# Kernel optimization log

Measured on AMD Instinct MI355X. Metric: run time of the kernel, lower is better.

## Reference

```python
import jax, jax.numpy as jnp
import numpy as np

M = 20000   # users
N = 20000   # items
E = 320000  # edges per channel per direction
C = 4       # channels
H = 4       # attention heads
D_IN = 256
D_OUT = 128
NEG_SLOPE = 0.01  # F.leaky_relu default


def setup_inputs() -> dict:
    key = jax.random.key(0)
    ks = jax.random.split(key, 12)
    u_prev = jax.random.normal(ks[0], (M, D_IN), jnp.float32)
    i_prev = jax.random.normal(ks[1], (N, D_IN), jnp.float32)
    # raw (pre-cumsum) shared parameters, 0.1*randn as in the module
    w_user = 0.1 * jax.random.normal(ks[2], (C, D_IN, D_OUT), jnp.float32)
    w_item = 0.1 * jax.random.normal(ks[3], (C, D_IN, D_OUT), jnp.float32)
    a_u_src = 0.1 * jax.random.normal(ks[4], (H, C, D_OUT), jnp.float32)
    a_u_dst = 0.1 * jax.random.normal(ks[5], (H, C, D_OUT), jnp.float32)
    a_i_src = 0.1 * jax.random.normal(ks[6], (H, C, D_OUT), jnp.float32)
    a_i_dst = 0.1 * jax.random.normal(ks[7], (H, C, D_OUT), jnp.float32)
    u2i_row = jax.random.randint(ks[8], (C, E), 0, M, jnp.int32)
    u2i_col = jax.random.randint(ks[9], (C, E), 0, N, jnp.int32)
    i2u_row = jax.random.randint(ks[10], (C, E), 0, N, jnp.int32)
    i2u_col = jax.random.randint(ks[11], (C, E), 0, M, jnp.int32)
    return dict(u_prev=u_prev, i_prev=i_prev, w_user=w_user, w_item=w_item,
                a_u_src=a_u_src, a_u_dst=a_u_dst, a_i_src=a_i_src, a_i_dst=a_i_dst,
                u2i_row=u2i_row, u2i_col=u2i_col, i2u_row=i2u_row, i2u_col=i2u_col)


def _segment_softmax(logits, seg, num_segments):
    # neighborhood softmax over edges grouped by destination row
    mx = jax.ops.segment_max(logits, seg, num_segments=num_segments)
    ex = jnp.exp(logits - mx[seg])
    den = jax.ops.segment_sum(ex, seg, num_segments=num_segments)
    return ex / den[seg]


def _attend(row, col, h_src, h_dst, a_src, a_dst, n_rows):
    # a_src, a_dst: (H, D_OUT). reduce_att = sum over heads; inner nonlinear = identity.
    # Node-level scores first (equivalent to gathering then dotting, much cheaper).
    s_src = h_src @ a_src.T  # (m, H)
    s_dst = h_dst @ a_dst.T  # (n, H)
    out = jnp.zeros((n_rows, h_dst.shape[1]), h_dst.dtype)
    for j in range(a_src.shape[0]):  # fixed small head loop
        logits = jax.nn.leaky_relu(s_src[row, j] + s_dst[col, j], NEG_SLOPE)  # (E,)
        att = _segment_softmax(logits, row, n_rows)                            # (E,)
        # sparse-dense matmul: out[r] += att_e * h_dst[c]
        out = out + jax.ops.segment_sum(att[:, None] * h_dst[col], row, num_segments=n_rows)
    return out


def reference(u_prev, i_prev, w_user, w_item, a_u_src, a_u_dst, a_i_src, a_i_dst,
              u2i_row, u2i_col, i2u_row, i2u_col):
    # SharedParameter[idx] = sum(xs[:idx+1]) -> cumulative sum along channel axis
    Wu = jnp.cumsum(w_user, axis=0)   # (C, D_IN, D_OUT)
    Wi = jnp.cumsum(w_item, axis=0)
    Aus = jnp.cumsum(a_u_src, axis=1)  # (H, C, D_OUT)
    Aud = jnp.cumsum(a_u_dst, axis=1)
    Ais = jnp.cumsum(a_i_src, axis=1)
    Aid = jnp.cumsum(a_i_dst, axis=1)

    u_outs, i_outs = [], []
    for c in range(C):
        u = u_prev @ Wu[c]  # (M, D_OUT), bias = 0 in MCGATLayer
        i = i_prev @ Wi[c]  # (N, D_OUT)
        u_next = _attend(u2i_row[c], u2i_col[c], u, i, Aus[:, c], Aud[:, c], M)
        i_next = _attend(i2u_row[c], i2u_col[c], i, u, Ais[:, c], Aid[:, c], N)
        u_outs.append(u_next)
        i_outs.append(i_next)

    # reduce_chnl == 'cat' (uniq_i = all nodes -> index_copy is identity placement)
    u_final = jax.nn.relu(jnp.concatenate(u_outs, axis=1))  # (M, C*D_OUT)
    i_final = jax.nn.relu(jnp.concatenate(i_outs, axis=1))  # (N, C*D_OUT)
    return (u_final, i_final)
```

## Files before the change

### kernel.cpp

```cpp
#include <hip/hip_runtime.h>
#include <math.h>

#define M_NODES 20000
#define MPAD    20096
#define NE      320000
#define NC      4
#define NH      4
#define DIN     256
#define DOUT    128
#define DCAT    512

#define RPB   256
#define NBKT  79
#define EPB   2048
#define NBLK  157
#define CAP   8192

typedef __attribute__((ext_vector_type(8))) _Float16 half8v;
typedef __attribute__((ext_vector_type(2))) _Float16 half2v;
typedef __attribute__((ext_vector_type(4))) float f32x4;

__device__ __forceinline__ unsigned short f2h(float x) {
    _Float16 h = (_Float16)x;
    return __builtin_bit_cast(unsigned short, h);
}
__device__ __forceinline__ void gload16(const void* g, void* l) {
    __builtin_amdgcn_global_load_lds(
        (const __attribute__((address_space(1))) void*)g,
        (__attribute__((address_space(3))) void*)l,
        16, 0, 0);
}

__global__ __launch_bounds__(256) void k_prep(const float* __restrict__ u_prev, const float* __restrict__ i_prev,
                                              const float* __restrict__ w_user, const float* __restrict__ w_item,
                                              const float* __restrict__ a_u_src, const float* __restrict__ a_u_dst,
                                              const float* __restrict__ a_i_src, const float* __restrict__ a_i_dst,
                                              const int* __restrict__ u2i_row, const int* __restrict__ i2u_row,
                                              unsigned short* __restrict__ AbU, unsigned short* __restrict__ AbI,
                                              unsigned short* __restrict__ BTu, unsigned short* __restrict__ BTi,
                                              unsigned short* __restrict__ Bvec, int* __restrict__ cnt3) {
    __shared__ int hist[NBKT];
    int bid = blockIdx.x, tid = threadIdx.x;
    if (bid < 5000) {
        int sideI = bid >= 2500;
        int t = (sideI ? bid - 2500 : bid) * 256 + tid;
        int row = t >> 5, kc = (t & 31) * 8;
        const float* src = sideI ? i_prev : u_prev;
        unsigned short* dst = sideI ? AbI : AbU;
        float4 x0 = *(const float4*)(src + (size_t)row * DIN + kc);
        float4 x1 = *(const float4*)(src + (size_t)row * DIN + kc + 4);
        float xs[8] = {x0.x, x0.y, x0.z, x0.w, x1.x, x1.y, x1.z, x1.w};
        unsigned int H[4];
#pragma unroll
        for (int p = 0; p < 4; ++p)
            H[p] = (unsigned int)f2h(xs[2 * p]) | ((unsigned int)f2h(xs[2 * p + 1]) << 16);
        *(uint4*)(dst + (size_t)row * 256 + kc) = make_uint4(H[0], H[1], H[2], H[3]);
        return;
    }
    if (bid < 6256) {
        int sub = bid - 5000;
        int combo = sub / NBLK, blk = sub % NBLK;
        int c = combo >> 1, dir = combo & 1;
        const int* rows = (dir ? i2u_row : u2i_row) + (size_t)c * NE;
        if (tid < NBKT) hist[tid] = 0;
        __syncthreads();
        int e0 = blk * EPB + tid * 8;
        if (e0 + 8 <= NE) {
            int4 r0 = *(const int4*)(rows + e0);
            int4 r1 = *(const int4*)(rows + e0 + 4);
            atomicAdd(&hist[r0.x >> 8], 1); atomicAdd(&hist[r0.y >> 8], 1);
            atomicAdd(&hist[r0.z >> 8], 1); atomicAdd(&hist[r0.w >> 8], 1);
            atomicAdd(&hist[r1.x >> 8], 1); atomicAdd(&hist[r1.y >> 8], 1);
            atomicAdd(&hist[r1.z >> 8], 1); atomicAdd(&hist[r1.w >> 8], 1);
        }
        __syncthreads();
        if (tid < NBKT) cnt3[((size_t)combo * NBKT + tid) * NBLK + blk] = hist[tid];
        return;
    }
    if (bid < 6384) {
        int idx = (bid - 6256) * 256 + tid;
        int k = idx >> 7, j = idx & 127;
        float su = 0.f, si = 0.f;
        for (int c = 0; c < NC; ++c) {
            su += w_user[((size_t)c * DIN + k) * DOUT + j];
            si += w_item[((size_t)c * DIN + k) * DOUT + j];
            size_t n = (size_t)(c * DOUT + j) * 256;
            BTu[n + k] = f2h(su);
            BTi[n + k] = f2h(si);
        }
        return;
    }
    {
        int t = (bid - 6384) * 256 + tid;
        int lane = t & 63, ks = (t >> 6) & 3, c = (t >> 8) & 3, side = t >> 10;
        int col = lane & 15, g = lane >> 4;
        int kind = (col >> 2) & 1, h = col & 3;
        const float* araw = kind ? (side ? a_u_dst : a_i_dst) : (side ? a_i_src : a_u_src);
        unsigned int out2[4];
#pragma unroll
        for (int p = 0; p < 4; ++p) {
            unsigned short e2[2];
#pragma unroll
            for (int q = 0; q < 2; ++q) {
                int j = p * 2 + q;
                int kdim = ks * 32 + g * 8 + j;
                float s = 0.f;
                if (col < 8)
                    for (int c2 = 0; c2 <= c; ++c2) s += araw[(h * NC + c2) * DOUT + kdim];
                e2[q] = f2h(s);
            }
            out2[p] = (unsigned int)e2[0] | ((unsigned int)e2[1] << 16);
        }
        *(uint4*)(Bvec + ((size_t)(((side * 4 + c) * 4 + ks) * 64 + lane)) * 8) =
            make_uint4(out2[0], out2[1], out2[2], out2[3]);
    }
}

__global__ __launch_bounds__(256) void k_gmm(const unsigned short* __restrict__ AbU,
                                             const unsigned short* __restrict__ AbI,
                                             const unsigned short* __restrict__ BTu,
                                             const unsigned short* __restrict__ BTi,
                                             const unsigned short* __restrict__ Bvec,
                                             unsigned short* __restrict__ fbu,
                                             unsigned short* __restrict__ fbi,
                                             float* __restrict__ su_src, float* __restrict__ su_dst,
                                             float* __restrict__ si_src, float* __restrict__ si_dst,
                                             int* __restrict__ cnt3, int* __restrict__ btot,
                                             int* __restrict__ bbase) {
    __shared__ unsigned short As[128 * 64];
    __shared__ unsigned short Bs[128 * 64];
    __shared__ int tot[128];
    int bid = blockIdx.x, tid = threadIdx.x;
    if (bid < 1256) {
        int side = bid >= 628;
        int t = side ? bid - 628 : bid;
        int c = t / 157, mb = t % 157;
        const unsigned short* Ab = side ? AbI : AbU;
        const unsigned short* BT = side ? BTi : BTu;
        unsigned short* fb       = side ? fbi : fbu;
        int m0 = mb * 128;
        int w = tid >> 6, lane = tid & 63;
        int wrb = (w >> 1) * 64, wcb = (w & 1) * 64;
        int l15 = lane & 15, g = lane >> 4;
        int srow = lane >> 3, scol = (lane & 7) * 8;
        f32x4 acc[4][4] = {};
        for (int kt = 0; kt < 4; ++kt) {
            int k0 = kt * 64;
#pragma unroll
            for (int tt = 0; tt < 4; ++tt) {
                int chunk = w * 4 + tt;
                int row8 = chunk * 8 + srow;
                gload16(Ab + (size_t)(m0 + row8) * 256 + k0 + scol, (char*)As + chunk * 1024);
                gload16(BT + (size_t)(c * 128 + row8) * 256 + k0 + scol, (char*)Bs + chunk * 1024);
            }
            __syncthreads();
#pragma unroll
            for (int ks = 0; ks < 2; ++ks) {
                half8v a[4], b[4];
#pragma unroll
                for (int i = 0; i < 4; ++i)
                    a[i] = *(const half8v*)(&As[(wrb + i * 16 + l15) * 64 + ks * 32 + g * 8]);
#pragma unroll
                for (int j = 0; j < 4; ++j)
                    b[j] = *(const half8v*)(&Bs[(wcb + j * 16 + l15) * 64 + ks * 32 + g * 8]);
#pragma unroll
                for (int i = 0; i < 4; ++i)
#pragma unroll
                    for (int j = 0; j < 4; ++j)
                        acc[i][j] = __builtin_amdgcn_mfma_f32_16x16x32_f16(a[i], b[j], acc[i][j], 0, 0, 0);
            }
            __syncthreads();
        }
#pragma unroll
        for (int i = 0; i < 4; ++i) {
#pragma unroll
            for (int r = 0; r < 4; ++r) {
                int nl = wrb + i * 16 + g * 4 + r;
                int node = m0 + nl;
                bool valid = node < M_NODES;
#pragma unroll
                for (int j = 0; j < 4; ++j) {
                    int d = wcb + j * 16 + l15;
                    unsigned short hv = f2h(acc[i][j][r]);
                    if (valid) fb[((size_t)c * M_NODES + node) * DOUT + d] = hv;
                    if (d < 64) As[nl * 64 + d] = hv;
                    else        Bs[nl * 64 + (d - 64)] = hv;
                }
            }
        }
        __syncthreads();
        {
            half8v bv[4];
#pragma unroll
            for (int ks = 0; ks < 4; ++ks)
                bv[ks] = *(const half8v*)(Bvec + ((size_t)(((side * 4 + c) * 4 + ks) * 64 + lane)) * 8);
#pragma unroll
            for (int mt2 = 0; mt2 < 2; ++mt2) {
                int mt = w * 2 + mt2;
                f32x4 sacc = {};
#pragma unroll
                for (int ks = 0; ks < 4; ++ks) {
                    int nl = mt * 16 + l15;
                    const unsigned short* base = (ks < 2) ? As : Bs;
                    half8v a = *(const half8v*)(&base[nl * 64 + (ks & 1) * 32 + g * 8]);
                    sacc = __builtin_amdgcn_mfma_f32_16x16x32_f16(a, bv[ks], sacc, 0, 0, 0);
                }
                int col = l15;
                if (col < 8) {
                    int kind = col >> 2, h = col & 3;
                    float* dst = kind ? (side ? si_dst : su_dst) : (side ? si_src : su_src);
#pragma unroll
                    for (int r = 0; r < 4; ++r) {
                        int node = m0 + mt * 16 + g * 4 + r;
                        if (node < M_NODES)
                            dst[((size_t)c * M_NODES + node) * 4 + h] = sacc[r];
                    }
                }
            }
        }
        return;
    }
    {
        int combo = bid - 1256;
        if (tid < NBKT) {
            size_t base = ((size_t)combo * NBKT + tid) * NBLK;
            int run = 0;
            for (int b = 0; b < NBLK; ++b) {
                int v = cnt3[base + b];
                cnt3[base + b] = run;
                run += v;
            }
            tot[tid] = run;
            btot[combo * NBKT + tid] = run;
        }
        __syncthreads();
        if (tid < 64) {
            int carry = 0;
            for (int ch = 0; ch < 2; ++ch) {
                int idx = ch * 64 + tid;
                int v = (idx < NBKT) ? tot[idx] : 0;
                int inc = v;
                for (int o = 1; o < 64; o <<= 1) {
                    int tv = __shfl_up(inc, o);
                    if (tid >= o) inc += tv;
                }
                if (idx < NBKT) bbase[combo * NBKT + idx] = carry + inc - v;
                carry += __shfl(inc, 63);
            }
        }
    }
}

__global__ __launch_bounds__(256) void k_bfill(const int* __restrict__ u2i_row, const int* __restrict__ u2i_col,
                                               const int* __restrict__ i2u_row, const int* __restrict__ i2u_col,
                                               const int* __restrict__ cnt3, const int* __restrict__ bbase,
                                               unsigned int* __restrict__ pairbuf) {
    __shared__ int cur[NBKT];
    int bid = blockIdx.x, tid = threadIdx.x;
    int combo = bid / NBLK, blk = bid % NBLK;
    int c = combo >> 1, dir = combo & 1;
    const int* rows = (dir ? i2u_row : u2i_row) + (size_t)c * NE;
    const int* cols = (dir ? i2u_col : u2i_col) + (size_t)c * NE;
    if (tid < NBKT)
        cur[tid] = bbase[combo * NBKT + tid] + cnt3[((size_t)combo * NBKT + tid) * NBLK + blk];
    __syncthreads();
    unsigned int* pb = pairbuf + (size_t)combo * NE;
    int e0 = blk * EPB + tid * 8;
    if (e0 + 8 <= NE) {
        int4 r0 = *(const int4*)(rows + e0);
        int4 r1 = *(const int4*)(rows + e0 + 4);
        int4 c0 = *(const int4*)(cols + e0);
        int4 c1 = *(const int4*)(cols + e0 + 4);
        int rr[8] = {r0.x, r0.y, r0.z, r0.w, r1.x, r1.y, r1.z, r1.w};
        int cc[8] = {c0.x, c0.y, c0.z, c0.w, c1.x, c1.y, c1.z, c1.w};
#pragma unroll
        for (int k = 0; k < 8; ++k) {
            int pos = atomicAdd(&cur[rr[k] >> 8], 1);
            pb[pos] = ((unsigned int)rr[k] << 16) | (unsigned int)cc[k];
        }
    }
}

__global__ __launch_bounds__(256) void k_finalize(const unsigned int* __restrict__ pairbuf,
                                                  const int* __restrict__ bbase, const int* __restrict__ btot,
                                                  int* __restrict__ csroff, int* __restrict__ csrcol) {
    __shared__ int hist[RPB];
    __shared__ int cur[RPB];
    __shared__ int lcol[CAP];
    int tid = threadIdx.x, bkt = blockIdx.x, combo = blockIdx.y;
    int base = bbase[combo * NBKT + bkt];
    int cntb = btot[combo * NBKT + bkt];
    const unsigned int* pb = pairbuf + (size_t)combo * NE + base;
    int* ccol = csrcol + (size_t)combo * NE + base;
    hist[tid] = 0;
    __syncthreads();
    for (int k = tid; k < cntb; k += 256)
        atomicAdd(&hist[(pb[k] >> 16) & (RPB - 1)], 1);
    __syncthreads();
    for (int st = 1; st < RPB; st <<= 1) {
        int v = (tid >= st) ? hist[tid - st] : 0;
        __syncthreads();
        hist[tid] += v;
        __syncthreads();
    }
    int ex = (tid == 0) ? 0 : hist[tid - 1];
    cur[tid] = ex;
    int row = bkt * RPB + tid;
    if (row < M_NODES) csroff[combo * (M_NODES + 1) + row] = base + ex;
    if (bkt == NBKT - 1 && tid == 0) csroff[combo * (M_NODES + 1) + M_NODES] = NE;
    __syncthreads();
    for (int k = tid; k < cntb; k += 256) {
        unsigned int p = pb[k];
        int rl  = (p >> 16) & (RPB - 1);
        int col = (int)(p & 0xffffu);
        int pos = atomicAdd(&cur[rl], 1);
        if (pos < CAP) lcol[pos] = col; else ccol[pos] = col;
    }
    __syncthreads();
    int lim = min(cntb, CAP);
    for (int k = tid; k < lim; k += 256) ccol[k] = lcol[k];
}

__device__ void attend_row_wave(int r, int s0, int deg, const float* __restrict__ ssrc,
                                const float* __restrict__ sdst, const unsigned short* __restrict__ fbd,
                                const int* __restrict__ co, float* __restrict__ o, int lane) {
    if (deg <= 64) {
        float w = 0.f;
        int cl = 0;
        if (deg > 0) {
            float4 ssv = *(const float4*)(ssrc + (size_t)r * 4);
            float ss[4] = {ssv.x, ssv.y, ssv.z, ssv.w};
            float lg[4];
            if (lane < deg) {
                cl = co[s0 + lane];
                float4 sdv = *(const float4*)(sdst + (size_t)cl * 4);
                float sd[4] = {sdv.x, sdv.y, sdv.z, sdv.w};
#pragma unroll
                for (int h = 0; h < 4; ++h) {
                    float x = ss[h] + sd[h];
                    lg[h] = x > 0.f ? x : 0.01f * x;
                }
            } else {
#pragma unroll
                for (int h = 0; h < 4; ++h) lg[h] = -1e30f;
            }
            float ex[4], den[4];
#pragma unroll
            for (int h = 0; h < 4; ++h) {
                ex[h] = __expf(fminf(lg[h], 80.f));
                den[h] = ex[h];
            }
#pragma unroll
            for (int h = 0; h < 4; ++h)
                for (int o2 = 32; o2; o2 >>= 1) den[h] += __shfl_xor(den[h], o2);
#pragma unroll
            for (int h = 0; h < 4; ++h) w += ex[h] * (1.f / den[h]);
        }
        int q = lane >> 4, l16 = lane & 15;
        const unsigned short* fbl = fbd + l16 * 8;
        float a8[8] = {};
        for (int j = 0; j < deg; j += 4) {
            int e = j + q;
            float we = __shfl(w, e & 63);
            int   ce = __shfl(cl, e & 63);
            if (e < deg) {
                half8v v = *(const half8v*)(fbl + (size_t)ce * DOUT);
#pragma unroll
                for (int k = 0; k < 8; ++k) a8[k] = fmaf(we, (float)v[k], a8[k]);
            }
        }
#pragma unroll
        for (int i = 0; i < 8; ++i) {
            a8[i] += __shfl_xor(a8[i], 16);
            a8[i] += __shfl_xor(a8[i], 32);
        }
        if (lane < 16) {
            float4 r0 = make_float4(fmaxf(a8[0], 0.f), fmaxf(a8[1], 0.f), fmaxf(a8[2], 0.f), fmaxf(a8[3], 0.f));
            float4 r1 = make_float4(fmaxf(a8[4], 0.f), fmaxf(a8[5], 0.f), fmaxf(a8[6], 0.f), fmaxf(a8[7], 0.f));
            *(float4*)(o + l16 * 8) = r0;
            *(float4*)(o + l16 * 8 + 4) = r1;
        }
        return;
    }
    float acc0 = 0.f, acc1 = 0.f;
    {
        float4 ssv = *(const float4*)(ssrc + (size_t)r * 4);
        float ss[4] = {ssv.x, ssv.y, ssv.z, ssv.w};
        float den[4] = {0.f, 0.f, 0.f, 0.f};
        for (int base = 0; base < deg; base += 64) {
            int e = base + lane;
            float ex[4] = {0.f, 0.f, 0.f, 0.f};
            if (e < deg) {
                int cl = co[s0 + e];
                float4 sdv = *(const float4*)(sdst + (size_t)cl * 4);
                float sd[4] = {sdv.x, sdv.y, sdv.z, sdv.w};
#pragma unroll
                for (int h = 0; h < 4; ++h) {
                    float x = ss[h] + sd[h];
                    x = x > 0.f ? x : 0.01f * x;
                    ex[h] = __expf(fminf(x, 80.f));
                }
            }
#pragma unroll
            for (int h = 0; h < 4; ++h) {
                float v = ex[h];
                for (int o2 = 32; o2; o2 >>= 1) v += __shfl_xor(v, o2);
                den[h] += v;
            }
        }
        float inv[4];
#pragma unroll
        for (int h = 0; h < 4; ++h) inv[h] = 1.f / den[h];
        for (int base = 0; base < deg; base += 64) {
            int e = base + lane;
            float w = 0.f;
            int cl = 0;
            if (e < deg) {
                cl = co[s0 + e];
                float4 sdv = *(const float4*)(sdst + (size_t)cl * 4);
                float sd[4] = {sdv.x, sdv.y, sdv.z, sdv.w};
#pragma unroll
                for (int h = 0; h < 4; ++h) {
                    float x = ss[h] + sd[h];
                    x = x > 0.f ? x : 0.01f * x;
                    w += __expf(fminf(x, 80.f)) * inv[h];
                }
            }
            int cnt2 = min(64, deg - base);
            for (int j = 0; j < cnt2; ++j) {
                float wj = __shfl(w, j);
                int   cj = __shfl(cl, j);
                half2v hv = *(const half2v*)(fbd + (size_t)cj * DOUT + lane * 2);
                acc0 = fmaf(wj, (float)hv[0], acc0);
                acc1 = fmaf(wj, (float)hv[1], acc1);
            }
        }
    }
    o[lane * 2]     = fmaxf(acc0, 0.f);
    o[lane * 2 + 1] = fmaxf(acc1, 0.f);
}

__global__ __launch_bounds__(256) void k_attend(const unsigned short* __restrict__ fbu, const unsigned short* __restrict__ fbi,
                                                const float* __restrict__ su_src, const float* __restrict__ su_dst,
                                                const float* __restrict__ si_src, const float* __restrict__ si_dst,
                                                const int* __restrict__ off, const int* __restrict__ cols,
                                                float* __restrict__ out) {
    int bid = blockIdx.x;
    int combo = bid & 7, c = combo >> 1, dir = combo & 1;
    int wavein = threadIdx.x >> 6, lane = threadIdx.x & 63;
    int half = lane >> 5, l = lane & 31;
    int rbase = (bid >> 3) * 8 + wavein * 2;
    const float* ssrc = (dir ? si_src : su_src) + (size_t)c * M_NODES * NH;
    const float* sdst = (dir ? su_dst : si_dst) + (size_t)c * M_NODES * NH;
    const unsigned short* fbd = (dir ? fbu : fbi) + (size_t)c * M_NODES * DOUT;
    const int* co = cols + (size_t)combo * NE;
    const int* offc = off + combo * (M_NODES + 1);
    int r = rbase + half;
    int s0 = offc[r];
    int deg = offc[r + 1] - s0;
    int degmax = max(deg, __shfl_xor(deg, 32));
    float* o = out + ((size_t)(dir ? M_NODES + r : r)) * DCAT + c * DOUT;

    if (degmax <= 32) {
        unsigned int pk = 0;
        if (deg > 0) {
            float w = 0.f;
            int cl = 0;
            float4 ssv = *(const float4*)(ssrc + (size_t)r * 4);
            float ss[4] = {ssv.x, ssv.y, ssv.z, ssv.w};
            float lg[4];
            if (l < deg) {
                cl = co[s0 + l];
                float4 sdv = *(const float4*)(sdst + (size_t)cl * 4);
                float sd[4] = {sdv.x, sdv.y, sdv.z, sdv.w};
#pragma unroll
                for (int h = 0; h < 4; ++h) {
                    float x = ss[h] + sd[h];
                    lg[h] = x > 0.f ? x : 0.01f * x;
                }
            } else {
#pragma unroll
                for (int h = 0; h < 4; ++h) lg[h] = -1e30f;
            }
            float ex[4], den[4];
#pragma unroll
            for (int h = 0; h < 4; ++h) {
                ex[h] = __expf(fminf(lg[h], 80.f));
                den[h] = ex[h];
            }
#pragma unroll
            for (int h = 0; h < 4; ++h)
                for (int o2 = 16; o2; o2 >>= 1) den[h] += __shfl_xor(den[h], o2);
#pragma unroll
            for (int h = 0; h < 4; ++h) w += ex[h] * (1.f / den[h]);
            pk = ((unsigned int)f2h(w) << 16) | (unsigned int)(cl & 0xffff);
        }
        int q2 = (l >> 4), l16 = l & 15;
        const char* fc = (const char*)(fbd + l16 * 8);
        half8v ah = {};
        int hb = half * 32;
        int j = 0;
        for (; j + 8 <= deg; j += 8) {
            unsigned int p0 = __shfl(pk, hb + j + q2);
            unsigned int p1 = __shfl(pk, hb + j + 2 + q2);
            unsigned int p2 = __shfl(pk, hb + j + 4 + q2);
            unsigned int p3 = __shfl(pk, hb + j + 6 + q2);
            half8v v0 = *(const half8v*)(fc + ((size_t)(p0 & 0xffffu) << 8));
            half8v v1 = *(const half8v*)(fc + ((size_t)(p1 & 0xffffu) << 8));
            half8v v2 = *(const half8v*)(fc + ((size_t)(p2 & 0xffffu) << 8));
            half8v v3 = *(const half8v*)(fc + ((size_t)(p3 & 0xffffu) << 8));
            ah += v0 * __builtin_bit_cast(_Float16, (unsigned short)(p0 >> 16));
            ah += v1 * __builtin_bit_cast(_Float16, (unsigned short)(p1 >> 16));
            ah += v2 * __builtin_bit_cast(_Float16, (unsigned short)(p2 >> 16));
            ah += v3 * __builtin_bit_cast(_Float16, (unsigned short)(p3 >> 16));
        }
        for (; j < deg; j += 4) {
            int e0 = j + q2, e1 = j + 2 + q2;
            unsigned int p0 = __shfl(pk, hb + min(e0, 31));
            unsigned int p1 = __shfl(pk, hb + min(e1, 31));
            p0 = (e0 < deg) ? p0 : 0u;
            p1 = (e1 < deg) ? p1 : 0u;
            half8v v0 = *(const half8v*)(fc + ((size_t)(p0 & 0xffffu) << 8));
            half8v v1 = *(const half8v*)(fc + ((size_t)(p1 & 0xffffu) << 8));
            ah += v0 * __builtin_bit_cast(_Float16, (unsigned short)(p0 >> 16));
            ah += v1 * __builtin_bit_cast(_Float16, (unsigned short)(p1 >> 16));
        }
        int4 ui = __builtin_bit_cast(int4, ah);
        int4 uo;
        uo.x = __shfl_xor(ui.x, 16);
        uo.y = __shfl_xor(ui.y, 16);
        uo.z = __shfl_xor(ui.z, 16);
        uo.w = __shfl_xor(ui.w, 16);
        ah += __builtin_bit_cast(half8v, uo);
        if (l < 16) {
            float4 r0 = make_float4(fmaxf((float)ah[0], 0.f), fmaxf((float)ah[1], 0.f),
                                    fmaxf((float)ah[2], 0.f), fmaxf((float)ah[3], 0.f));
            float4 r1 = make_float4(fmaxf((float)ah[4], 0.f), fmaxf((float)ah[5], 0.f),
                                    fmaxf((float)ah[6], 0.f), fmaxf((float)ah[7], 0.f));
            *(float4*)(o + l16 * 8) = r0;
            *(float4*)(o + l16 * 8 + 4) = r1;
        }
        return;
    }

    for (int rr = 0; rr < 2; ++rr) {
        int r2 = rbase + rr;
        int t0 = offc[r2];
        int d2 = offc[r2 + 1] - t0;
        float* o2 = out + ((size_t)(dir ? M_NODES + r2 : r2)) * DCAT + c * DOUT;
        attend_row_wave(r2, t0, d2, ssrc, sdst, fbd, co, o2, lane);
    }
}

extern "C" void kernel_launch(void* const* d_in, const int* in_sizes, int n_in,
                              void* d_out, int out_size, void* d_ws, size_t ws_size,
                              hipStream_t stream) {
    const float* u_prev  = (const float*)d_in[0];
    const float* i_prev  = (const float*)d_in[1];
    const float* w_user  = (const float*)d_in[2];
    const float* w_item  = (const float*)d_in[3];
    const float* a_u_src = (const float*)d_in[4];
    const float* a_u_dst = (const float*)d_in[5];
    const float* a_i_src = (const float*)d_in[6];
    const float* a_i_dst = (const float*)d_in[7];
    const int* u2i_row = (const int*)d_in[8];
    const int* u2i_col = (const int*)d_in[9];
    const int* i2u_row = (const int*)d_in[10];
    const int* i2u_col = (const int*)d_in[11];
    float* out = (float*)d_out;

    char* ws = (char*)d_ws;
    size_t woff = 0;
    auto alloc = [&](size_t bytes) -> char* {
        char* p = ws + woff;
        woff += (bytes + 255) & ~(size_t)255;
        return p;
    };
    unsigned short* AbU   = (unsigned short*)alloc((size_t)MPAD * 256 * 2);
    unsigned short* AbI   = (unsigned short*)alloc((size_t)MPAD * 256 * 2);
    unsigned short* BTu   = (unsigned short*)alloc((size_t)512 * 256 * 2);
    unsigned short* BTi   = (unsigned short*)alloc((size_t)512 * 256 * 2);
    unsigned short* Bvec  = (unsigned short*)alloc((size_t)2 * 4 * 4 * 64 * 8 * 2);
    unsigned short* fbu   = (unsigned short*)alloc((size_t)NC * M_NODES * DOUT * 2);
    unsigned short* fbi   = (unsigned short*)alloc((size_t)NC * M_NODES * DOUT * 2);
    float* su_src = (float*)alloc((size_t)NC * M_NODES * NH * 4);
    float* su_dst = (float*)alloc((size_t)NC * M_NODES * NH * 4);
    float* si_src = (float*)alloc((size_t)NC * M_NODES * NH * 4);
    float* si_dst = (float*)alloc((size_t)NC * M_NODES * NH * 4);
    int* csroff   = (int*)alloc((size_t)8 * (M_NODES + 1) * 4);
    int* csrcol   = (int*)alloc((size_t)8 * NE * 4);
    int* cnt3     = (int*)alloc((size_t)8 * NBKT * NBLK * 4);
    int* btot     = (int*)alloc((size_t)8 * NBKT * 4);
    int* bbase    = (int*)alloc((size_t)8 * NBKT * 4);
    unsigned int* pairbuf = (unsigned int*)alloc((size_t)8 * NE * 4);

    k_prep<<<6392, 256, 0, stream>>>(u_prev, i_prev, w_user, w_item,
                                     a_u_src, a_u_dst, a_i_src, a_i_dst,
                                     u2i_row, i2u_row,
                                     AbU, AbI, BTu, BTi, Bvec, cnt3);
    k_gmm<<<1264, 256, 0, stream>>>(AbU, AbI, BTu, BTi, Bvec, fbu, fbi,
                                    su_src, su_dst, si_src, si_dst,
                                    cnt3, btot, bbase);
    k_bfill<<<1256, 256, 0, stream>>>(u2i_row, u2i_col, i2u_row, i2u_col,
                                      cnt3, bbase, pairbuf);
    k_finalize<<<dim3(NBKT, 8), 256, 0, stream>>>(pairbuf, bbase, btot, csroff, csrcol);
    k_attend<<<dim3(M_NODES * 8 / 8), 256, 0, stream>>>(fbu, fbi, su_src, su_dst,
                                                        si_src, si_dst, csroff, csrcol, out);
}
```

Before: 143.3 us.

## Fuse CSR finalize into attention kernel with smaller row buckets held in LDS

Shrinks the row buckets from 256 to 64 rows, giving 313 buckets, and merges the finalize and attend kernels into one. Each block now builds its bucket's per-row column lists in shared memory and runs attention directly from LDS, so the csroff/csrcol arrays are never written to or read back from global memory. This removes one launch and a round-trip through global memory. The costs are more histogram buckets and scan work in the earlier kernels, and any bucket with more than 4096 edges would lose the overflowing columns because there is no spill path.

```diff
diff --git a/kernel.cpp b/kernel.cpp
--- a/kernel.cpp
+++ b/kernel.cpp
@@ -10,11 +10,11 @@
 #define DOUT    128
 #define DCAT    512
 
-#define RPB   256
-#define NBKT  79
+#define RPB2  64
+#define NBKT2 313
 #define EPB   2048
 #define NBLK  157
-#define CAP   8192
+#define CAP2  4096
 
 typedef __attribute__((ext_vector_type(8))) _Float16 half8v;
 typedef __attribute__((ext_vector_type(2))) _Float16 half2v;
@@ -39,7 +39,7 @@
                                               unsigned short* __restrict__ AbU, unsigned short* __restrict__ AbI,
                                               unsigned short* __restrict__ BTu, unsigned short* __restrict__ BTi,
                                               unsigned short* __restrict__ Bvec, int* __restrict__ cnt3) {
-    __shared__ int hist[NBKT];
+    __shared__ int hist[NBKT2];
     int bid = blockIdx.x, tid = threadIdx.x;
     if (bid < 5000) {
         int sideI = bid >= 2500;
@@ -62,19 +62,20 @@
         int combo = sub / NBLK, blk = sub % NBLK;
         int c = combo >> 1, dir = combo & 1;
         const int* rows = (dir ? i2u_row : u2i_row) + (size_t)c * NE;
-        if (tid < NBKT) hist[tid] = 0;
+        for (int i = tid; i < NBKT2; i += 256) hist[i] = 0;
         __syncthreads();
         int e0 = blk * EPB + tid * 8;
         if (e0 + 8 <= NE) {
             int4 r0 = *(const int4*)(rows + e0);
             int4 r1 = *(const int4*)(rows + e0 + 4);
-            atomicAdd(&hist[r0.x >> 8], 1); atomicAdd(&hist[r0.y >> 8], 1);
-            atomicAdd(&hist[r0.z >> 8], 1); atomicAdd(&hist[r0.w >> 8], 1);
-            atomicAdd(&hist[r1.x >> 8], 1); atomicAdd(&hist[r1.y >> 8], 1);
-            atomicAdd(&hist[r1.z >> 8], 1); atomicAdd(&hist[r1.w >> 8], 1);
+            atomicAdd(&hist[r0.x >> 6], 1); atomicAdd(&hist[r0.y >> 6], 1);
+            atomicAdd(&hist[r0.z >> 6], 1); atomicAdd(&hist[r0.w >> 6], 1);
+            atomicAdd(&hist[r1.x >> 6], 1); atomicAdd(&hist[r1.y >> 6], 1);
+            atomicAdd(&hist[r1.z >> 6], 1); atomicAdd(&hist[r1.w >> 6], 1);
         }
         __syncthreads();
-        if (tid < NBKT) cnt3[((size_t)combo * NBKT + tid) * NBLK + blk] = hist[tid];
+        for (int i = tid; i < NBKT2; i += 256)
+            cnt3[((size_t)combo * NBKT2 + i) * NBLK + blk] = hist[i];
         return;
     }
     if (bid < 6384) {
@@ -129,7 +130,7 @@
                                              int* __restrict__ bbase) {
     __shared__ unsigned short As[128 * 64];
     __shared__ unsigned short Bs[128 * 64];
-    __shared__ int tot[128];
+    __shared__ int tot[NBKT2];
     int bid = blockIdx.x, tid = threadIdx.x;
     if (bid < 1256) {
         int side = bid >= 628;
@@ -222,29 +223,29 @@
     }
     {
         int combo = bid - 1256;
-        if (tid < NBKT) {
-            size_t base = ((size_t)combo * NBKT + tid) * NBLK;
+        for (int bkt = tid; bkt < NBKT2; bkt += 256) {
+            size_t basep = ((size_t)combo * NBKT2 + bkt) * NBLK;
             int run = 0;
             for (int b = 0; b < NBLK; ++b) {
-                int v = cnt3[base + b];
-                cnt3[base + b] = run;
+                int v = cnt3[basep + b];
+                cnt3[basep + b] = run;
                 run += v;
             }
-            tot[tid] = run;
-            btot[combo * NBKT + tid] = run;
+            tot[bkt] = run;
+            btot[combo * NBKT2 + bkt] = run;
         }
         __syncthreads();
         if (tid < 64) {
             int carry = 0;
-            for (int ch = 0; ch < 2; ++ch) {
+            for (int ch = 0; ch < 5; ++ch) {
                 int idx = ch * 64 + tid;
-                int v = (idx < NBKT) ? tot[idx] : 0;
+                int v = (idx < NBKT2) ? tot[idx] : 0;
                 int inc = v;
                 for (int o = 1; o < 64; o <<= 1) {
                     int tv = __shfl_up(inc, o);
                     if (tid >= o) inc += tv;
                 }
-                if (idx < NBKT) bbase[combo * NBKT + idx] = carry + inc - v;
+                if (idx < NBKT2) bbase[combo * NBKT2 + idx] = carry + inc - v;
                 carry += __shfl(inc, 63);
             }
         }
@@ -255,14 +256,14 @@
                                                const int* __restrict__ i2u_row, const int* __restrict__ i2u_col,
                                                const int* __restrict__ cnt3, const int* __restrict__ bbase,
                                                unsigned int* __restrict__ pairbuf) {
-    __shared__ int cur[NBKT];
+    __shared__ int cur[NBKT2];
     int bid = blockIdx.x, tid = threadIdx.x;
     int combo = bid / NBLK, blk = bid % NBLK;
     int c = combo >> 1, dir = combo & 1;
     const int* rows = (dir ? i2u_row : u2i_row) + (size_t)c * NE;
     const int* cols = (dir ? i2u_col : u2i_col) + (size_t)c * NE;
-    if (tid < NBKT)
-        cur[tid] = bbase[combo * NBKT + tid] + cnt3[((size_t)combo * NBKT + tid) * NBLK + blk];
+    for (int i = tid; i < NBKT2; i += 256)
+        cur[i] = bbase[combo * NBKT2 + i] + cnt3[((size_t)combo * NBKT2 + i) * NBLK + blk];
     __syncthreads();
     unsigned int* pb = pairbuf + (size_t)combo * NE;
     int e0 = blk * EPB + tid * 8;
@@ -275,55 +276,15 @@
         int cc[8] = {c0.x, c0.y, c0.z, c0.w, c1.x, c1.y, c1.z, c1.w};
 #pragma unroll
         for (int k = 0; k < 8; ++k) {
-            int pos = atomicAdd(&cur[rr[k] >> 8], 1);
+            int pos = atomicAdd(&cur[rr[k] >> 6], 1);
             pb[pos] = ((unsigned int)rr[k] << 16) | (unsigned int)cc[k];
         }
     }
-}
-
-__global__ __launch_bounds__(256) void k_finalize(const unsigned int* __restrict__ pairbuf,
-                                                  const int* __restrict__ bbase, const int* __restrict__ btot,
-                                                  int* __restrict__ csroff, int* __restrict__ csrcol) {
-    __shared__ int hist[RPB];
-    __shared__ int cur[RPB];
-    __shared__ int lcol[CAP];
-    int tid = threadIdx.x, bkt = blockIdx.x, combo = blockIdx.y;
-    int base = bbase[combo * NBKT + bkt];
-    int cntb = btot[combo * NBKT + bkt];
-    const unsigned int* pb = pairbuf + (size_t)combo * NE + base;
-    int* ccol = csrcol + (size_t)combo * NE + base;
-    hist[tid] = 0;
-    __syncthreads();
-    for (int k = tid; k < cntb; k += 256)
-        atomicAdd(&hist[(pb[k] >> 16) & (RPB - 1)], 1);
-    __syncthreads();
-    for (int st = 1; st < RPB; st <<= 1) {
-        int v = (tid >= st) ? hist[tid - st] : 0;
-        __syncthreads();
-        hist[tid] += v;
-        __syncthreads();
-    }
-    int ex = (tid == 0) ? 0 : hist[tid - 1];
-    cur[tid] = ex;
-    int row = bkt * RPB + tid;
-    if (row < M_NODES) csroff[combo * (M_NODES + 1) + row] = base + ex;
-    if (bkt == NBKT - 1 && tid == 0) csroff[combo * (M_NODES + 1) + M_NODES] = NE;
-    __syncthreads();
-    for (int k = tid; k < cntb; k += 256) {
-        unsigned int p = pb[k];
-        int rl  = (p >> 16) & (RPB - 1);
-        int col = (int)(p & 0xffffu);
-        int pos = atomicAdd(&cur[rl], 1);
-        if (pos < CAP) lcol[pos] = col; else ccol[pos] = col;
-    }
-    __syncthreads();
-    int lim = min(cntb, CAP);
-    for (int k = tid; k < lim; k += 256) ccol[k] = lcol[k];
 }
 
 __device__ void attend_row_wave(int r, int s0, int deg, const float* __restrict__ ssrc,
                                 const float* __restrict__ sdst, const unsigned short* __restrict__ fbd,
-                                const int* __restrict__ co, float* __restrict__ o, int lane) {
+                                const int* co, float* __restrict__ o, int lane) {
     if (deg <= 64) {
         float w = 0.f;
         int cl = 0;
@@ -440,115 +401,148 @@
     o[lane * 2 + 1] = fmaxf(acc1, 0.f);
 }
 
-__global__ __launch_bounds__(256) void k_attend(const unsigned short* __restrict__ fbu, const unsigned short* __restrict__ fbi,
-                                                const float* __restrict__ su_src, const float* __restrict__ su_dst,
-                                                const float* __restrict__ si_src, const float* __restrict__ si_dst,
-                                                const int* __restrict__ off, const int* __restrict__ cols,
-                                                float* __restrict__ out) {
-    int bid = blockIdx.x;
-    int combo = bid & 7, c = combo >> 1, dir = combo & 1;
-    int wavein = threadIdx.x >> 6, lane = threadIdx.x & 63;
-    int half = lane >> 5, l = lane & 31;
-    int rbase = (bid >> 3) * 8 + wavein * 2;
+__global__ __launch_bounds__(256) void k_fat(const unsigned int* __restrict__ pairbuf,
+                                             const int* __restrict__ bbase, const int* __restrict__ btot,
+                                             const unsigned short* __restrict__ fbu,
+                                             const unsigned short* __restrict__ fbi,
+                                             const float* __restrict__ su_src, const float* __restrict__ su_dst,
+                                             const float* __restrict__ si_src, const float* __restrict__ si_dst,
+                                             float* __restrict__ out) {
+    __shared__ int hist[RPB2];
+    __shared__ int cur[RPB2];
+    __shared__ int lcol[CAP2];
+    int tid = threadIdx.x, bid = blockIdx.x;
+    int combo = bid & 7, bkt = bid >> 3;
+    int c = combo >> 1, dir = combo & 1;
+    int base = bbase[combo * NBKT2 + bkt];
+    int cntb = btot[combo * NBKT2 + bkt];
+    const unsigned int* pb = pairbuf + (size_t)combo * NE + base;
+    if (tid < RPB2) hist[tid] = 0;
+    __syncthreads();
+    for (int k = tid; k < cntb; k += 256)
+        atomicAdd(&hist[(pb[k] >> 16) & (RPB2 - 1)], 1);
+    __syncthreads();
+    if (tid < 64) {
+        int v = hist[tid];
+        int inc = v;
+        for (int o = 1; o < 64; o <<= 1) {
+            int t = __shfl_up(inc, o);
+            if (tid >= o) inc += t;
+        }
+        hist[tid] = inc;
+        cur[tid] = inc - v;
+    }
+    __syncthreads();
+    for (int k = tid; k < cntb; k += 256) {
+        unsigned int p = pb[k];
+        int rl  = (p >> 16) & (RPB2 - 1);
+        int pos = atomicAdd(&cur[rl], 1);
+        if (pos < CAP2) lcol[pos] = (int)(p & 0xffffu);
+    }
+    __syncthreads();
     const float* ssrc = (dir ? si_src : su_src) + (size_t)c * M_NODES * NH;
     const float* sdst = (dir ? su_dst : si_dst) + (size_t)c * M_NODES * NH;
     const unsigned short* fbd = (dir ? fbu : fbi) + (size_t)c * M_NODES * DOUT;
-    const int* co = cols + (size_t)combo * NE;
-    const int* offc = off + combo * (M_NODES + 1);
-    int r = rbase + half;
-    int s0 = offc[r];
-    int deg = offc[r + 1] - s0;
-    int degmax = max(deg, __shfl_xor(deg, 32));
-    float* o = out + ((size_t)(dir ? M_NODES + r : r)) * DCAT + c * DOUT;
-
-    if (degmax <= 32) {
-        unsigned int pk = 0;
-        if (deg > 0) {
-            float w = 0.f;
-            int cl = 0;
-            float4 ssv = *(const float4*)(ssrc + (size_t)r * 4);
-            float ss[4] = {ssv.x, ssv.y, ssv.z, ssv.w};
-            float lg[4];
-            if (l < deg) {
-                cl = co[s0 + l];
-                float4 sdv = *(const float4*)(sdst + (size_t)cl * 4);
-                float sd[4] = {sdv.x, sdv.y, sdv.z, sdv.w};
+    int wavein = tid >> 6, lane = tid & 63;
+    int half = lane >> 5, l = lane & 31;
+    for (int iter = 0; iter < 8; ++iter) {
+        int rloc = iter * 8 + wavein * 2 + half;
+        int r = bkt * RPB2 + rloc;
+        int start = rloc ? hist[rloc - 1] : 0;
+        int deg = hist[rloc] - start;
+        int degmax = max(deg, __shfl_xor(deg, 32));
+        bool valid = r < M_NODES;
+        float* o = out + ((size_t)(dir ? M_NODES + r : r)) * DCAT + c * DOUT;
+        if (degmax <= 32) {
+            unsigned int pk = 0;
+            if (deg > 0) {
+                float w = 0.f;
+                int cl = 0;
+                float4 ssv = *(const float4*)(ssrc + (size_t)r * 4);
+                float ss[4] = {ssv.x, ssv.y, ssv.z, ssv.w};
+                float lg[4];
+                if (l < deg) {
+                    cl = lcol[start + l];
+                    float4 sdv = *(const float4*)(sdst + (size_t)cl * 4);
+                    float sd[4] = {sdv.x, sdv.y, sdv.z, sdv.w};
+#pragma unroll
+                    for (int h = 0; h < 4; ++h) {
+                        float x = ss[h] + sd[h];
+                        lg[h] = x > 0.f ? x : 0.01f * x;
+                    }
+                } else {
+#pragma unroll
+                    for (int h = 0; h < 4; ++h) lg[h] = -1e30f;
+                }
+                float ex[4], den[4];
 #pragma unroll
                 for (int h = 0; h < 4; ++h) {
-                    float x = ss[h] + sd[h];
-                    lg[h] = x > 0.f ? x : 0.01f * x;
-                }
-            } else {
-#pragma unroll
-                for (int h = 0; h < 4; ++h) lg[h] = -1e30f;
-            }
-            float ex[4], den[4];
-#pragma unroll
-            for (int h = 0; h < 4; ++h) {
-                ex[h] = __expf(fminf(lg[h], 80.f));
-                den[h] = ex[h];
-            }
-#pragma unroll
-            for (int h = 0; h < 4; ++h)
-                for (int o2 = 16; o2; o2 >>= 1) den[h] += __shfl_xor(den[h], o2);
-#pragma unroll
-            for (int h = 0; h < 4; ++h) w += ex[h] * (1.f / den[h]);
-            pk = ((unsigned int)f2h(w) << 16) | (unsigned int)(cl & 0xffff);
-        }
-        int q2 = (l >> 4), l16 = l & 15;
-        const char* fc = (const char*)(fbd + l16 * 8);
-        half8v ah = {};
-        int hb = half * 32;
-        int j = 0;
-        for (; j + 8 <= deg; j += 8) {
-            unsigned int p0 = __shfl(pk, hb + j + q2);
-            unsigned int p1 = __shfl(pk, hb + j + 2 + q2);
-            unsigned int p2 = __shfl(pk, hb + j + 4 + q2);
-            unsigned int p3 = __shfl(pk, hb + j + 6 + q2);
-            half8v v0 = *(const half8v*)(fc + ((size_t)(p0 & 0xffffu) << 8));
-            half8v v1 = *(const half8v*)(fc + ((size_t)(p1 & 0xffffu) << 8));
-            half8v v2 = *(const half8v*)(fc + ((size_t)(p2 & 0xffffu) << 8));
-            half8v v3 = *(const half8v*)(fc + ((size_t)(p3 & 0xffffu) << 8));
-            ah += v0 * __builtin_bit_cast(_Float16, (unsigned short)(p0 >> 16));
-            ah += v1 * __builtin_bit_cast(_Float16, (unsigned short)(p1 >> 16));
-            ah += v2 * __builtin_bit_cast(_Float16, (unsigned short)(p2 >> 16));
-            ah += v3 * __builtin_bit_cast(_Float16, (unsigned short)(p3 >> 16));
-        }
-        for (; j < deg; j += 4) {
-            int e0 = j + q2, e1 = j + 2 + q2;
-            unsigned int p0 = __shfl(pk, hb + min(e0, 31));
-            unsigned int p1 = __shfl(pk, hb + min(e1, 31));
-            p0 = (e0 < deg) ? p0 : 0u;
-            p1 = (e1 < deg) ? p1 : 0u;
-            half8v v0 = *(const half8v*)(fc + ((size_t)(p0 & 0xffffu) << 8));
-            half8v v1 = *(const half8v*)(fc + ((size_t)(p1 & 0xffffu) << 8));
-            ah += v0 * __builtin_bit_cast(_Float16, (unsigned short)(p0 >> 16));
-            ah += v1 * __builtin_bit_cast(_Float16, (unsigned short)(p1 >> 16));
-        }
-        int4 ui = __builtin_bit_cast(int4, ah);
-        int4 uo;
-        uo.x = __shfl_xor(ui.x, 16);
-        uo.y = __shfl_xor(ui.y, 16);
-        uo.z = __shfl_xor(ui.z, 16);
-        uo.w = __shfl_xor(ui.w, 16);
-        ah += __builtin_bit_cast(half8v, uo);
-        if (l < 16) {
-            float4 r0 = make_float4(fmaxf((float)ah[0], 0.f), fmaxf((float)ah[1], 0.f),
-                                    fmaxf((float)ah[2], 0.f), fmaxf((float)ah[3], 0.f));
-            float4 r1 = make_float4(fmaxf((float)ah[4], 0.f), fmaxf((float)ah[5], 0.f),
-                                    fmaxf((float)ah[6], 0.f), fmaxf((float)ah[7], 0.f));
-            *(float4*)(o + l16 * 8) = r0;
-            *(float4*)(o + l16 * 8 + 4) = r1;
-        }
-        return;
-    }
-
-    for (int rr = 0; rr < 2; ++rr) {
-        int r2 = rbase + rr;
-        int t0 = offc[r2];
-        int d2 = offc[r2 + 1] - t0;
-        float* o2 = out + ((size_t)(dir ? M_NODES + r2 : r2)) * DCAT + c * DOUT;
-        attend_row_wave(r2, t0, d2, ssrc, sdst, fbd, co, o2, lane);
+                    ex[h] = __expf(fminf(lg[h], 80.f));
+                    den[h] = ex[h];
+                }
+#pragma unroll
+                for (int h = 0; h < 4; ++h)
+                    for (int o2 = 16; o2; o2 >>= 1) den[h] += __shfl_xor(den[h], o2);
+#pragma unroll
+                for (int h = 0; h < 4; ++h) w += ex[h] * (1.f / den[h]);
+                pk = ((unsigned int)f2h(w) << 16) | (unsigned int)(cl & 0xffff);
+            }
+            int q2 = (l >> 4), l16 = l & 15;
+            const char* fc = (const char*)(fbd + l16 * 8);
+            half8v ah = {};
+            int hb = half * 32;
+            int j = 0;
+            for (; j + 8 <= deg; j += 8) {
+                unsigned int p0 = __shfl(pk, hb + j + q2);
+                unsigned int p1 = __shfl(pk, hb + j + 2 + q2);
+                unsigned int p2 = __shfl(pk, hb + j + 4 + q2);
+                unsigned int p3 = __shfl(pk, hb + j + 6 + q2);
+                half8v v0 = *(const half8v*)(fc + ((size_t)(p0 & 0xffffu) << 8));
+                half8v v1 = *(const half8v*)(fc + ((size_t)(p1 & 0xffffu) << 8));
+                half8v v2 = *(const half8v*)(fc + ((size_t)(p2 & 0xffffu) << 8));
+                half8v v3 = *(const half8v*)(fc + ((size_t)(p3 & 0xffffu) << 8));
+                ah += v0 * __builtin_bit_cast(_Float16, (unsigned short)(p0 >> 16));
+                ah += v1 * __builtin_bit_cast(_Float16, (unsigned short)(p1 >> 16));
+                ah += v2 * __builtin_bit_cast(_Float16, (unsigned short)(p2 >> 16));
+                ah += v3 * __builtin_bit_cast(_Float16, (unsigned short)(p3 >> 16));
+            }
+            for (; j < deg; j += 4) {
+                int e0 = j + q2, e1 = j + 2 + q2;
+                unsigned int p0 = __shfl(pk, hb + min(e0, 31));
+                unsigned int p1 = __shfl(pk, hb + min(e1, 31));
+                p0 = (e0 < deg) ? p0 : 0u;
+                p1 = (e1 < deg) ? p1 : 0u;
+                half8v v0 = *(const half8v*)(fc + ((size_t)(p0 & 0xffffu) << 8));
+                half8v v1 = *(const half8v*)(fc + ((size_t)(p1 & 0xffffu) << 8));
+                ah += v0 * __builtin_bit_cast(_Float16, (unsigned short)(p0 >> 16));
+                ah += v1 * __builtin_bit_cast(_Float16, (unsigned short)(p1 >> 16));
+            }
+            int4 ui = __builtin_bit_cast(int4, ah);
+            int4 uo;
+            uo.x = __shfl_xor(ui.x, 16);
+            uo.y = __shfl_xor(ui.y, 16);
+            uo.z = __shfl_xor(ui.z, 16);
+            uo.w = __shfl_xor(ui.w, 16);
+            ah += __builtin_bit_cast(half8v, uo);
+            if (valid && l < 16) {
+                float4 r0 = make_float4(fmaxf((float)ah[0], 0.f), fmaxf((float)ah[1], 0.f),
+                                        fmaxf((float)ah[2], 0.f), fmaxf((float)ah[3], 0.f));
+                float4 r1 = make_float4(fmaxf((float)ah[4], 0.f), fmaxf((float)ah[5], 0.f),
+                                        fmaxf((float)ah[6], 0.f), fmaxf((float)ah[7], 0.f));
+                *(float4*)(o + l16 * 8) = r0;
+                *(float4*)(o + l16 * 8 + 4) = r1;
+            }
+        } else {
+            for (int rr = 0; rr < 2; ++rr) {
+                int rloc2 = iter * 8 + wavein * 2 + rr;
+                int r2 = bkt * RPB2 + rloc2;
+                if (r2 >= M_NODES) continue;
+                int st2 = rloc2 ? hist[rloc2 - 1] : 0;
+                int d2 = hist[rloc2] - st2;
+                float* o2 = out + ((size_t)(dir ? M_NODES + r2 : r2)) * DCAT + c * DOUT;
+                attend_row_wave(r2, st2, d2, ssrc, sdst, fbd, lcol, o2, lane);
+            }
+        }
     }
 }
 
@@ -587,11 +581,9 @@
     float* su_dst = (float*)alloc((size_t)NC * M_NODES * NH * 4);
     float* si_src = (float*)alloc((size_t)NC * M_NODES * NH * 4);
     float* si_dst = (float*)alloc((size_t)NC * M_NODES * NH * 4);
-    int* csroff   = (int*)alloc((size_t)8 * (M_NODES + 1) * 4);
-    int* csrcol   = (int*)alloc((size_t)8 * NE * 4);
-    int* cnt3     = (int*)alloc((size_t)8 * NBKT * NBLK * 4);
-    int* btot     = (int*)alloc((size_t)8 * NBKT * 4);
-    int* bbase    = (int*)alloc((size_t)8 * NBKT * 4);
+    int* cnt3     = (int*)alloc((size_t)8 * NBKT2 * NBLK * 4);
+    int* btot     = (int*)alloc((size_t)8 * NBKT2 * 4);
+    int* bbase    = (int*)alloc((size_t)8 * NBKT2 * 4);
     unsigned int* pairbuf = (unsigned int*)alloc((size_t)8 * NE * 4);
 
     k_prep<<<6392, 256, 0, stream>>>(u_prev, i_prev, w_user, w_item,
@@ -603,7 +595,6 @@
                                     cnt3, btot, bbase);
     k_bfill<<<1256, 256, 0, stream>>>(u2i_row, u2i_col, i2u_row, i2u_col,
                                       cnt3, bbase, pairbuf);
-    k_finalize<<<dim3(NBKT, 8), 256, 0, stream>>>(pairbuf, bbase, btot, csroff, csrcol);
-    k_attend<<<dim3(M_NODES * 8 / 8), 256, 0, stream>>>(fbu, fbi, su_src, su_dst,
-                                                        si_src, si_dst, csroff, csrcol, out);
-}
+    k_fat<<<NBKT2 * 8, 256, 0, stream>>>(pairbuf, bbase, btot, fbu, fbi,
+                                         su_src, su_dst, si_src, si_dst, out);
+}
```

New measurement: 175.0 us. 22.1% more time.

## Swizzle GEMM LDS tiles and parallelize bucket-count scans across wavefronts

Applied to the files above, without the earlier changes.

The GEMM's shared-memory tiles now use an XOR swizzle on 16-byte column chunks, applied consistently to the global-to-LDS loads, the MFMA operand reads and the epilogue reuse, to cut LDS bank conflicts. The per-bucket sequential exclusive scan over 157 block counts, which ran on one thread per bucket, is replaced by extra blocks that do a wavefront shuffle scan per (combo, bucket) into a new cpre buffer. The bucket totals are computed separately with unrolled sums. The cost is one more buffer, more launched blocks, and the totals being read twice from cnt3.

```diff
diff --git a/kernel.cpp b/kernel.cpp
--- a/kernel.cpp
+++ b/kernel.cpp
@@ -125,11 +125,10 @@
                                              unsigned short* __restrict__ fbi,
                                              float* __restrict__ su_src, float* __restrict__ su_dst,
                                              float* __restrict__ si_src, float* __restrict__ si_dst,
-                                             int* __restrict__ cnt3, int* __restrict__ btot,
-                                             int* __restrict__ bbase) {
+                                             const int* __restrict__ cnt3, int* __restrict__ cpre,
+                                             int* __restrict__ btot, int* __restrict__ bbase) {
     __shared__ unsigned short As[128 * 64];
     __shared__ unsigned short Bs[128 * 64];
-    __shared__ int tot[128];
     int bid = blockIdx.x, tid = threadIdx.x;
     if (bid < 1256) {
         int side = bid >= 628;
@@ -142,7 +141,8 @@
         int w = tid >> 6, lane = tid & 63;
         int wrb = (w >> 1) * 64, wcb = (w & 1) * 64;
         int l15 = lane & 15, g = lane >> 4;
-        int srow = lane >> 3, scol = (lane & 7) * 8;
+        int srow = lane >> 3;
+        int scolSwz = (((lane & 7) ^ srow)) * 8;
         f32x4 acc[4][4] = {};
         for (int kt = 0; kt < 4; ++kt) {
             int k0 = kt * 64;
@@ -150,19 +150,25 @@
             for (int tt = 0; tt < 4; ++tt) {
                 int chunk = w * 4 + tt;
                 int row8 = chunk * 8 + srow;
-                gload16(Ab + (size_t)(m0 + row8) * 256 + k0 + scol, (char*)As + chunk * 1024);
-                gload16(BT + (size_t)(c * 128 + row8) * 256 + k0 + scol, (char*)Bs + chunk * 1024);
+                gload16(Ab + (size_t)(m0 + row8) * 256 + k0 + scolSwz, (char*)As + chunk * 1024);
+                gload16(BT + (size_t)(c * 128 + row8) * 256 + k0 + scolSwz, (char*)Bs + chunk * 1024);
             }
             __syncthreads();
 #pragma unroll
             for (int ks = 0; ks < 2; ++ks) {
                 half8v a[4], b[4];
 #pragma unroll
-                for (int i = 0; i < 4; ++i)
-                    a[i] = *(const half8v*)(&As[(wrb + i * 16 + l15) * 64 + ks * 32 + g * 8]);
-#pragma unroll
-                for (int j = 0; j < 4; ++j)
-                    b[j] = *(const half8v*)(&Bs[(wcb + j * 16 + l15) * 64 + ks * 32 + g * 8]);
+                for (int i = 0; i < 4; ++i) {
+                    int row = wrb + i * 16 + l15;
+                    int colSwz = (((ks * 4 + g) ^ (row & 7))) * 8;
+                    a[i] = *(const half8v*)(&As[row * 64 + colSwz]);
+                }
+#pragma unroll
+                for (int j = 0; j < 4; ++j) {
+                    int row = wcb + j * 16 + l15;
+                    int colSwz = (((ks * 4 + g) ^ (row & 7))) * 8;
+                    b[j] = *(const half8v*)(&Bs[row * 64 + colSwz]);
+                }
 #pragma unroll
                 for (int i = 0; i < 4; ++i)
 #pragma unroll
@@ -178,13 +184,14 @@
                 int nl = wrb + i * 16 + g * 4 + r;
                 int node = m0 + nl;
                 bool valid = node < M_NODES;
+                int sw = (nl & 7) * 8;
 #pragma unroll
                 for (int j = 0; j < 4; ++j) {
                     int d = wcb + j * 16 + l15;
                     unsigned short hv = f2h(acc[i][j][r]);
                     if (valid) fb[((size_t)c * M_NODES + node) * DOUT + d] = hv;
-                    if (d < 64) As[nl * 64 + d] = hv;
-                    else        Bs[nl * 64 + (d - 64)] = hv;
+                    if (d < 64) As[nl * 64 + (d ^ sw)] = hv;
+                    else        Bs[nl * 64 + ((d - 64) ^ sw)] = hv;
                 }
             }
         }
@@ -202,7 +209,9 @@
                 for (int ks = 0; ks < 4; ++ks) {
                     int nl = mt * 16 + l15;
                     const unsigned short* base = (ks < 2) ? As : Bs;
-                    half8v a = *(const half8v*)(&base[nl * 64 + (ks & 1) * 32 + g * 8]);
+                    int col = (ks & 1) * 32 + g * 8;
+                    int colSwz = col ^ ((nl & 7) * 8);
+                    half8v a = *(const half8v*)(&base[nl * 64 + colSwz]);
                     sacc = __builtin_amdgcn_mfma_f32_16x16x32_f16(a, bv[ks], sacc, 0, 0, 0);
                 }
                 int col = l15;
@@ -220,18 +229,43 @@
         }
         return;
     }
+    if (bid < 1414) {
+        int w = tid >> 6, lane = tid & 63;
+        int wid = (bid - 1256) * 4 + w;
+        int combo = wid & 7, bkt = wid >> 3;
+        size_t base = ((size_t)combo * NBKT + bkt) * NBLK;
+        int carry = 0;
+#pragma unroll
+        for (int ch = 0; ch < 3; ++ch) {
+            int idx = ch * 64 + lane;
+            int v = (idx < NBLK) ? cnt3[base + idx] : 0;
+            int inc = v;
+            for (int o = 1; o < 64; o <<= 1) {
+                int tv = __shfl_up(inc, o);
+                if (lane >= o) inc += tv;
+            }
+            if (idx < NBLK) cpre[base + idx] = carry + inc - v;
+            carry += __shfl(inc, 63);
+        }
+        return;
+    }
     {
-        int combo = bid - 1256;
-        if (tid < NBKT) {
-            size_t base = ((size_t)combo * NBKT + tid) * NBLK;
-            int run = 0;
-            for (int b = 0; b < NBLK; ++b) {
-                int v = cnt3[base + b];
-                cnt3[base + b] = run;
-                run += v;
-            }
-            tot[tid] = run;
-            btot[combo * NBKT + tid] = run;
+        int combo = bid - 1414;
+        int* tot = (int*)As;
+        for (int bkt = tid; bkt < NBKT; bkt += 256) {
+            size_t base = ((size_t)combo * NBKT + bkt) * NBLK;
+            int s0 = 0, s1 = 0, s2 = 0, s3 = 0;
+            int b = 0;
+            for (; b + 4 <= NBLK; b += 4) {
+                s0 += cnt3[base + b];
+                s1 += cnt3[base + b + 1];
+                s2 += cnt3[base + b + 2];
+                s3 += cnt3[base + b + 3];
+            }
+            for (; b < NBLK; ++b) s0 += cnt3[base + b];
+            int s = s0 + s1 + s2 + s3;
+            tot[bkt] = s;
+            btot[combo * NBKT + bkt] = s;
         }
         __syncthreads();
         if (tid < 64) {
@@ -253,7 +287,7 @@
 
 __global__ __launch_bounds__(256) void k_bfill(const int* __restrict__ u2i_row, const int* __restrict__ u2i_col,
                                                const int* __restrict__ i2u_row, const int* __restrict__ i2u_col,
-                                               const int* __restrict__ cnt3, const int* __restrict__ bbase,
+                                               const int* __restrict__ cpre, const int* __restrict__ bbase,
                                                unsigned int* __restrict__ pairbuf) {
     __shared__ int cur[NBKT];
     int bid = blockIdx.x, tid = threadIdx.x;
@@ -262,7 +296,7 @@
     const int* rows = (dir ? i2u_row : u2i_row) + (size_t)c * NE;
     const int* cols = (dir ? i2u_col : u2i_col) + (size_t)c * NE;
     if (tid < NBKT)
-        cur[tid] = bbase[combo * NBKT + tid] + cnt3[((size_t)combo * NBKT + tid) * NBLK + blk];
+        cur[tid] = bbase[combo * NBKT + tid] + cpre[((size_t)combo * NBKT + tid) * NBLK + blk];
     __syncthreads();
     unsigned int* pb = pairbuf + (size_t)combo * NE;
     int e0 = blk * EPB + tid * 8;
@@ -590,6 +624,7 @@
     int* csroff   = (int*)alloc((size_t)8 * (M_NODES + 1) * 4);
     int* csrcol   = (int*)alloc((size_t)8 * NE * 4);
     int* cnt3     = (int*)alloc((size_t)8 * NBKT * NBLK * 4);
+    int* cpre     = (int*)alloc((size_t)8 * NBKT * NBLK * 4);
     int* btot     = (int*)alloc((size_t)8 * NBKT * 4);
     int* bbase    = (int*)alloc((size_t)8 * NBKT * 4);
     unsigned int* pairbuf = (unsigned int*)alloc((size_t)8 * NE * 4);
@@ -598,11 +633,11 @@
                                      a_u_src, a_u_dst, a_i_src, a_i_dst,
                                      u2i_row, i2u_row,
                                      AbU, AbI, BTu, BTi, Bvec, cnt3);
-    k_gmm<<<1264, 256, 0, stream>>>(AbU, AbI, BTu, BTi, Bvec, fbu, fbi,
+    k_gmm<<<1422, 256, 0, stream>>>(AbU, AbI, BTu, BTi, Bvec, fbu, fbi,
                                     su_src, su_dst, si_src, si_dst,
-                                    cnt3, btot, bbase);
+                                    cnt3, cpre, btot, bbase);
     k_bfill<<<1256, 256, 0, stream>>>(u2i_row, u2i_col, i2u_row, i2u_col,
-                                      cnt3, bbase, pairbuf);
+                                      cpre, bbase, pairbuf);
     k_finalize<<<dim3(NBKT, 8), 256, 0, stream>>>(pairbuf, bbase, btot, csroff, csrcol);
     k_attend<<<dim3(M_NODES * 8 / 8), 256, 0, stream>>>(fbu, fbi, su_src, su_dst,
                                                         si_src, si_dst, csroff, csrcol, out);
```

After: 134.2 us. 1.07x faster.
